# Performance work log

Hardware: AMD Instinct MI355X
Metric: run time of the kernel (lower is better)

The kernel has to match this reference:

```python
import jax, jax.numpy as jnp
import numpy as np
import math

B, L, E, H = 4, 2048, 1024, 16
HD = E // H
SIGMA = 10.0
ATTN_BIAS = 0.1  # source bug: dropout_p=0.1 is passed as attn_mask and added to scores


def setup_inputs() -> dict:
    key = jax.random.key(0)
    ks = jax.random.split(key, 6)
    return {
        "query": jax.random.normal(ks[0], (B, L, E), jnp.float32),
        "key": jax.random.normal(ks[1], (B, L, E), jnp.float32),
        "value": jax.random.normal(ks[2], (B, L, E), jnp.float32),
        "gauss": jax.random.uniform(ks[3], (B * H // 2, L), jnp.float32),
        "in_proj_weight": jax.random.normal(ks[4], (3 * E, E), jnp.float32) * (1.0 / math.sqrt(E)),
        "in_proj_bias": jnp.zeros((3 * E,), jnp.float32),
        "out_proj_weight": jax.random.normal(ks[5], (E, E), jnp.float32) * (1.0 / math.sqrt(E)),
        "out_proj_bias": jnp.zeros((E,), jnp.float32),
    }


def reference(query, key, value, gauss, in_proj_weight, in_proj_bias,
              out_proj_weight, out_proj_bias):
    # packed in-projection (q,k,v distinct tensors -> chunk weights in 3)
    wq, wk, wv = jnp.split(in_proj_weight, 3, axis=0)   # each [E, E]
    bq, bk, bv = jnp.split(in_proj_bias, 3, axis=0)
    q = query @ wq.T + bq          # [B, L, E]
    k = key @ wk.T + bk
    v = value @ wv.T + bv

    def split_heads(x):            # [B, L, E] -> [B*H, L, HD], index = b*H + h
        return x.reshape(B, L, H, HD).transpose(0, 2, 1, 3).reshape(B * H, L, HD)

    q, k, v = split_heads(q), split_heads(k), split_heads(v)
    q = q * (1.0 / math.sqrt(HD))

    attn = jnp.einsum("bnd,bmd->bnm", q, k) + ATTN_BIAS   # [B*H, L, L]
    gw = jnp.exp(-gauss * SIGMA)                          # [B*H//2, L]
    # even/odd batch rows share the same gaussian row -> pairwise broadcast
    attn = (attn.reshape(B * H // 2, 2, L, L) * gw[:, None, None, :]).reshape(B * H, L, L)
    attn = jax.nn.softmax(attn, axis=-1)

    out = jnp.einsum("bnm,bmd->bnd", attn, v)             # [B*H, L, HD]
    out = out.reshape(B, H, L, HD).transpose(0, 2, 1, 3).reshape(B, L, E)
    return out @ out_proj_weight.T + out_proj_bias        # [B, L, E]
```

## Files before the change

kernel.cpp:

```cpp
#include <hip/hip_runtime.h>
#include <stdint.h>
#include <stddef.h>


typedef __attribute__((ext_vector_type(8))) short bf16x8;
typedef __attribute__((ext_vector_type(4))) float f32x4;
typedef __attribute__((ext_vector_type(8))) float f32x8;

__device__ __forceinline__ unsigned short f2b(float f) {
  unsigned int u = __builtin_bit_cast(unsigned int, f);
  u += 0x7FFFu + ((u >> 16) & 1u);
  return (unsigned short)(u >> 16);
}
__device__ __forceinline__ bf16x8 cvt8(f32x4 a, f32x4 b) {
  bf16x8 r;
#pragma unroll
  for (int i = 0; i < 4; ++i) { r[i] = (short)f2b(a[i]); r[4 + i] = (short)f2b(b[i]); }
  return r;
}
__device__ __forceinline__ bf16x8 pk8(f32x4 a, f32x4 b) {
  union { bf16x8 v; unsigned int w[4]; } u;
  asm("v_cvt_pk_bf16_f32 %0, %1, %2" : "=v"(u.w[0]) : "v"(a[0]), "v"(a[1]));
  asm("v_cvt_pk_bf16_f32 %0, %1, %2" : "=v"(u.w[1]) : "v"(a[2]), "v"(a[3]));
  asm("v_cvt_pk_bf16_f32 %0, %1, %2" : "=v"(u.w[2]) : "v"(b[0]), "v"(b[1]));
  asm("v_cvt_pk_bf16_f32 %0, %1, %2" : "=v"(u.w[3]) : "v"(b[2]), "v"(b[3]));
  return u.v;
}
__device__ __forceinline__ float fexp2(float x) { return __builtin_amdgcn_exp2f(x); }

#define GLD16(gp, lp) __builtin_amdgcn_global_load_lds( \
  (const __attribute__((address_space(1))) void*)(gp), \
  (__attribute__((address_space(3))) void*)(lp), 16, 0, 0)

__global__ void __launch_bounds__(256) gw_exp_kernel(const float* __restrict__ g,
                                                     float* __restrict__ gw2, int n) {
  int i = blockIdx.x * 256 + threadIdx.x;
  if (i < n) {
    const float e = __expf(g[i] * -10.0f) * 1.44269504f;
    gw2[2 * i] = e;
    gw2[2 * i + 1] = 0.1f * e;
  }
}

__global__ void __launch_bounds__(256) conv_bf16_kernel(
    const float* __restrict__ q, const float* __restrict__ k, const float* __restrict__ v,
    const float* __restrict__ w1, const float* __restrict__ w2,
    unsigned short* __restrict__ dst)
{
  const size_t i = ((size_t)blockIdx.x * 256 + threadIdx.x) * 8;
  const int seg = (int)(i >> 20);
  const float* s; size_t off;
  if (seg < 8)       { s = q;  off = i; }
  else if (seg < 16) { s = k;  off = i - ((size_t)8 << 20); }
  else if (seg < 24) { s = v;  off = i - ((size_t)16 << 20); }
  else if (seg < 27) { s = w1; off = i - ((size_t)24 << 20); }
  else               { s = w2; off = i - ((size_t)27 << 20); }
  const f32x4 a = *(const f32x4*)(s + off);
  const f32x4 b = *(const f32x4*)(s + off + 4);
  *(bf16x8*)(dst + i) = cvt8(a, b);
}

template<int EPI>
__global__ void __launch_bounds__(256) gemm_bt(
    const unsigned short* __restrict__ A0, const unsigned short* __restrict__ Bw,
    const float* __restrict__ bias,
    unsigned short* __restrict__ Qo, unsigned short* __restrict__ Ko,
    unsigned short* __restrict__ Vto, float* __restrict__ Co,
    int N, int K, int nTN)
{
  const int nwg = gridDim.x;
  const int cpx = nwg >> 3;
  const int bid2 = (blockIdx.x & 7) * cpx + (blockIdx.x >> 3);
  const int tm = bid2 / nTN, tn = bid2 % nTN;

  const unsigned short* A = A0;
  if (EPI == 0) A = A0 + (size_t)(tn >> 3) * 8388608;

  __shared__ __align__(16) char ldsA[3][8192];
  __shared__ __align__(16) char ldsB[3][8192];

  const int tid = threadIdx.x;
  const int w = tid >> 6, l = tid & 63;
  const int lr = l & 15, lg = l >> 4;
  const size_t Kz = (size_t)K;

  auto stage = [&](int buf, int kt) {
    const int k0 = kt * 32;
    const int rl = l >> 2;
    const int cs = (l & 3) ^ ((l >> 3) & 3);
#pragma unroll
    for (int i = 0; i < 2; ++i) {
      const int s = i * 4 + w;
      const size_t row = (size_t)(s * 16 + rl);
      GLD16(A  + (Kz * (tm * 128 + row)) + k0 + cs * 8, &ldsA[buf][s * 1024]);
      GLD16(Bw + (Kz * (tn * 128 + row)) + k0 + cs * 8, &ldsB[buf][s * 1024]);
    }
  };

  auto loadFrag = [&](const char* ld, int row) -> bf16x8 {
    return *(const bf16x8*)(ld + row * 64 + ((lg ^ ((row >> 1) & 3)) << 4));
  };

  f32x4 acc[4][4];
  const f32x4 zero = {0.f, 0.f, 0.f, 0.f};
#pragma unroll
  for (int i = 0; i < 4; ++i)
#pragma unroll
    for (int j = 0; j < 4; ++j) acc[i][j] = zero;

  const int wr = (w >> 1) * 64, wc = (w & 1) * 64;
  const int NT = K / 32;

  stage(0, 0);
  stage(1, 1);
  int rb = 0, wb = 2;
  for (int kt = 0; kt < NT; ++kt) {
    if (kt == NT - 1) { asm volatile("s_waitcnt vmcnt(0)" ::: "memory"); }
    else              { asm volatile("s_waitcnt vmcnt(4)" ::: "memory"); }
    __builtin_amdgcn_sched_barrier(0);
    __builtin_amdgcn_s_barrier();
    __builtin_amdgcn_sched_barrier(0);
    if (kt + 2 < NT) stage(wb, kt + 2);
    const char* la = ldsA[rb];
    const char* lb = ldsB[rb];
    bf16x8 af[4], bfr[4];
#pragma unroll
    for (int mi = 0; mi < 4; ++mi) af[mi] = loadFrag(la, wr + mi * 16 + lr);
#pragma unroll
    for (int ni = 0; ni < 4; ++ni) bfr[ni] = loadFrag(lb, wc + ni * 16 + lr);
#pragma unroll
    for (int mi = 0; mi < 4; ++mi)
#pragma unroll
      for (int ni = 0; ni < 4; ++ni)
        acc[mi][ni] = __builtin_amdgcn_mfma_f32_16x16x32_bf16(
            af[mi], bfr[ni], acc[mi][ni], 0, 0, 0);
    rb = (rb == 2) ? 0 : rb + 1;
    wb = (wb == 2) ? 0 : wb + 1;
  }

#pragma unroll
  for (int ni = 0; ni < 4; ++ni) {
    const int cn = tn * 128 + wc + ni * 16 + lr;
    const float bv = bias[cn];
#pragma unroll
    for (int mi = 0; mi < 4; ++mi) {
#pragma unroll
      for (int r = 0; r < 4; ++r) {
        const int rm = tm * 128 + wr + mi * 16 + lg * 4 + r;
        const float val = acc[mi][ni][r] + bv;
        if constexpr (EPI == 0) {
          const int which = cn >> 10;
          const int j = cn & 1023;
          const int bh = (rm >> 11) * 16 + (j >> 6);
          const int d = j & 63;
          const int n = rm & 2047;
          if (which == 0)      Qo[((size_t)bh * 2048 + n) * 64 + d] = f2b(val * 0.125f);
          else if (which == 1) Ko[((size_t)bh * 2048 + n) * 64 + d] = f2b(val);
          else                 Vto[((size_t)bh * 64 + d) * 2048 + n] = f2b(val);
        } else {
          Co[(size_t)rm * N + cn] = val;
        }
      }
    }
  }
}

__global__ void __launch_bounds__(256, 4) attn_kernel(
    const unsigned short* __restrict__ Q, const unsigned short* __restrict__ Kf,
    const unsigned short* __restrict__ Vt, const float* __restrict__ gw2,
    unsigned short* __restrict__ O)
{
  const int bh = blockIdx.x >> 4;
  const int qb = blockIdx.x & 15;
  const int tid = threadIdx.x;
  const int w = tid >> 6, l = tid & 63;
  const int lr = l & 15, lg = l >> 4;

  __shared__ __align__(16) unsigned short Kl[2][64 * 64];
  __shared__ __align__(16) unsigned short Vl[2][64 * 64];

  const int qrow = qb * 128 + w * 32 + lr;
  const unsigned short* qp = &Q[((size_t)bh * 2048 + qrow) * 64];
  const bf16x8 aqA0 = *(const bf16x8*)&qp[lg * 8];
  const bf16x8 aqA1 = *(const bf16x8*)&qp[32 + lg * 8];
  const bf16x8 aqB0 = *(const bf16x8*)&qp[16 * 64 + lg * 8];
  const bf16x8 aqB1 = *(const bf16x8*)&qp[16 * 64 + 32 + lg * 8];

  const f32x4 zero = {0.f, 0.f, 0.f, 0.f};
  f32x4 accOA[4], accOB[4], lA = zero, lB = zero;
#pragma unroll
  for (int dt = 0; dt < 4; ++dt) { accOA[dt] = zero; accOB[dt] = zero; }

  const short oneb = (short)0x3F80;
  const bf16x8 vones = {oneb, oneb, oneb, oneb, oneb, oneb, oneb, oneb};

  int off[4][2];
#pragma unroll
  for (int mt = 0; mt < 4; ++mt)
#pragma unroll
    for (int c = 0; c < 2; ++c) {
      const int rr = mt * 16 + lr;
      off[mt][c] = rr * 128 + ((((c << 2) + lg) ^ (rr & 7)) << 4);
    }

  const int rr0 = w * 8 + (l >> 3);
  const int cc = ((l & 7) ^ (rr0 & 7)) * 8;
  const int kk0 = (rr0 & 35) | ((rr0 & 12) << 1) | ((rr0 & 16) >> 2);
  const unsigned short* kSrc = &Kf[((size_t)bh * 2048 + kk0) * 64 + cc];
  const unsigned short* vSrc = &Vt[((size_t)bh * 64 + rr0) * 2048 + cc];

  auto stageKV = [&](int buf) {
    GLD16(kSrc,             &Kl[buf][w * 512]);
    GLD16(kSrc + 32 * 64,   &Kl[buf][(w + 4) * 512]);
    GLD16(vSrc,             &Vl[buf][w * 512]);
    GLD16(vSrc + 32 * 2048, &Vl[buf][(w + 4) * 512]);
    kSrc += 64 * 64;
    vSrc += 64;
  };

  const float* gwrow = &gw2[(size_t)(bh >> 1) * 4096];

  stageKV(0);
  for (int t = 0; t < 32; ++t) {
    __syncthreads();
    if (t + 1 < 32) stageKV((t + 1) & 1);
    const char* kl = (const char*)Kl[t & 1];
    const char* vl = (const char*)Vl[t & 1];

    f32x4 s0[4], s1[4];
    __builtin_amdgcn_s_setprio(1);
#pragma unroll
    for (int mt = 0; mt < 4; ++mt) {
      f32x4 a0 = zero, a1 = zero;
#pragma unroll
      for (int dk = 0; dk < 2; ++dk) {
        const bf16x8 bk = *(const bf16x8*)(kl + off[mt][dk]);
        a0 = __builtin_amdgcn_mfma_f32_16x16x32_bf16(bk, dk ? aqA1 : aqA0, a0, 0, 0, 0);
        a1 = __builtin_amdgcn_mfma_f32_16x16x32_bf16(bk, dk ? aqB1 : aqB0, a1, 0, 0, 0);
      }
      const f32x8 g8 = *(const f32x8*)(gwrow + ((t << 7) + ((mt >> 1) << 6) + ((mt & 1) << 3) + (lg << 4)));
#pragma unroll
      for (int r = 0; r < 4; ++r) {
        s0[mt][r] = __builtin_fmaf(a0[r], g8[2 * r], g8[2 * r + 1]);
        s1[mt][r] = __builtin_fmaf(a1[r], g8[2 * r], g8[2 * r + 1]);
      }
    }
    __builtin_amdgcn_s_setprio(0);

#pragma unroll
    for (int mt = 0; mt < 4; ++mt)
#pragma unroll
      for (int r = 0; r < 4; ++r) {
        s0[mt][r] = fexp2(s0[mt][r]);
        s1[mt][r] = fexp2(s1[mt][r]);
      }
    const bf16x8 apA0 = pk8(s0[0], s0[1]);
    const bf16x8 apA1 = pk8(s0[2], s0[3]);
    const bf16x8 apB0 = pk8(s1[0], s1[1]);
    const bf16x8 apB1 = pk8(s1[2], s1[3]);

    __builtin_amdgcn_s_setprio(1);
    lA = __builtin_amdgcn_mfma_f32_16x16x32_bf16(apA0, vones, lA, 0, 0, 0);
    lA = __builtin_amdgcn_mfma_f32_16x16x32_bf16(apA1, vones, lA, 0, 0, 0);
    lB = __builtin_amdgcn_mfma_f32_16x16x32_bf16(apB0, vones, lB, 0, 0, 0);
    lB = __builtin_amdgcn_mfma_f32_16x16x32_bf16(apB1, vones, lB, 0, 0, 0);

#pragma unroll
    for (int dt = 0; dt < 4; ++dt) {
      f32x4 a = accOA[dt], b = accOB[dt];
#pragma unroll
      for (int ms = 0; ms < 2; ++ms) {
        const bf16x8 bv = *(const bf16x8*)(vl + off[dt][ms]);
        a = __builtin_amdgcn_mfma_f32_16x16x32_bf16(ms ? apA1 : apA0, bv, a, 0, 0, 0);
        b = __builtin_amdgcn_mfma_f32_16x16x32_bf16(ms ? apB1 : apB0, bv, b, 0, 0, 0);
      }
      accOA[dt] = a; accOB[dt] = b;
    }
    __builtin_amdgcn_s_setprio(0);
  }

  const int orowA = (bh >> 4) * 2048 + qb * 128 + w * 32 + lg * 4;
  const int oc0 = (bh & 15) * 64;
  f32x4 rA, rB;
#pragma unroll
  for (int r = 0; r < 4; ++r) { rA[r] = 1.0f / lA[r]; rB[r] = 1.0f / lB[r]; }
#pragma unroll
  for (int dt = 0; dt < 4; ++dt) {
#pragma unroll
    for (int r = 0; r < 4; ++r) {
      O[(size_t)(orowA + r) * 1024 + oc0 + dt * 16 + lr]      = f2b(accOA[dt][r] * rA[r]);
      O[(size_t)(orowA + 16 + r) * 1024 + oc0 + dt * 16 + lr] = f2b(accOB[dt][r] * rB[r]);
    }
  }
}

extern "C" void kernel_launch(void* const* d_in, const int* in_sizes, int n_in,
                              void* d_out, int out_size, void* d_ws, size_t ws_size,
                              hipStream_t stream) {
  (void)in_sizes; (void)n_in; (void)out_size; (void)ws_size;
  const float* query = (const float*)d_in[0];
  const float* key_  = (const float*)d_in[1];
  const float* value = (const float*)d_in[2];
  const float* gauss = (const float*)d_in[3];
  const float* ipw   = (const float*)d_in[4];
  const float* ipb   = (const float*)d_in[5];
  const float* opw   = (const float*)d_in[6];
  const float* opb   = (const float*)d_in[7];

  char* ws = (char*)d_ws;
  unsigned short* Xbf = (unsigned short*)ws;
  unsigned short* W1  = Xbf + ((size_t)24 << 20);
  unsigned short* W2  = Xbf + ((size_t)27 << 20);
  unsigned short* AO  = Xbf;
  unsigned short* Qf  = Xbf + ((size_t)28 << 20);
  unsigned short* Kf  = Qf + (size_t)64 * 2048 * 64;
  unsigned short* Vt  = Kf + (size_t)64 * 2048 * 64;
  float*          gw2 = (float*)(Vt + (size_t)64 * 2048 * 64);

  gw_exp_kernel<<<256, 256, 0, stream>>>(gauss, gw2, 32 * 2048);

  conv_bf16_kernel<<<14336, 256, 0, stream>>>(query, key_, value, ipw, opw, Xbf);

  gemm_bt<0><<<64 * 24, 256, 0, stream>>>(
      Xbf, W1, ipb, Qf, Kf, Vt, nullptr, 3072, 1024, 24);

  attn_kernel<<<64 * 16, 256, 0, stream>>>(Qf, Kf, Vt, gw2, AO);

  gemm_bt<1><<<64 * 8, 256, 0, stream>>>(
      AO, W2, opb, nullptr, nullptr, nullptr, (float*)d_out, 1024, 1024, 8);
}
```

Before: 230.8 us.

## Use 512-thread GEMM blocks and stage V-transpose epilogue through LDS

The projection GEMMs now launch 512 threads (8 waves) per 128x128 tile, so each wave computes a 64x32 sub-tile and issues one global-to-LDS load per operand per stage instead of two. A and B tiles share a single LDS array. For the V part of the input projection, the epilogue writes bias-added bf16 results transposed into swizzled LDS, then emits coalesced 16-byte stores to the transposed V layout in place of scattered 2-byte strided stores. The tradeoff is fewer accumulators per wave and less fragment reuse, plus extra barriers in the V epilogue.

```diff
diff --git a/kernel.cpp b/kernel.cpp
--- a/kernel.cpp
+++ b/kernel.cpp
@@ -61,7 +61,7 @@
 }
 
 template<int EPI>
-__global__ void __launch_bounds__(256) gemm_bt(
+__global__ void __launch_bounds__(512) gemm_bt(
     const unsigned short* __restrict__ A0, const unsigned short* __restrict__ Bw,
     const float* __restrict__ bias,
     unsigned short* __restrict__ Qo, unsigned short* __restrict__ Ko,
@@ -76,8 +76,7 @@
   const unsigned short* A = A0;
   if (EPI == 0) A = A0 + (size_t)(tn >> 3) * 8388608;
 
-  __shared__ __align__(16) char ldsA[3][8192];
-  __shared__ __align__(16) char ldsB[3][8192];
+  __shared__ __align__(16) char lds[3][16384];
 
   const int tid = threadIdx.x;
   const int w = tid >> 6, l = tid & 63;
@@ -88,27 +87,23 @@
     const int k0 = kt * 32;
     const int rl = l >> 2;
     const int cs = (l & 3) ^ ((l >> 3) & 3);
-#pragma unroll
-    for (int i = 0; i < 2; ++i) {
-      const int s = i * 4 + w;
-      const size_t row = (size_t)(s * 16 + rl);
-      GLD16(A  + (Kz * (tm * 128 + row)) + k0 + cs * 8, &ldsA[buf][s * 1024]);
-      GLD16(Bw + (Kz * (tn * 128 + row)) + k0 + cs * 8, &ldsB[buf][s * 1024]);
-    }
+    const size_t row = (size_t)(w * 16 + rl);
+    GLD16(A  + Kz * (tm * 128 + row) + k0 + cs * 8, &lds[buf][w * 1024]);
+    GLD16(Bw + Kz * (tn * 128 + row) + k0 + cs * 8, &lds[buf][8192 + w * 1024]);
   };
 
   auto loadFrag = [&](const char* ld, int row) -> bf16x8 {
     return *(const bf16x8*)(ld + row * 64 + ((lg ^ ((row >> 1) & 3)) << 4));
   };
 
-  f32x4 acc[4][4];
+  f32x4 acc[4][2];
   const f32x4 zero = {0.f, 0.f, 0.f, 0.f};
 #pragma unroll
   for (int i = 0; i < 4; ++i)
 #pragma unroll
-    for (int j = 0; j < 4; ++j) acc[i][j] = zero;
-
-  const int wr = (w >> 1) * 64, wc = (w & 1) * 64;
+    for (int j = 0; j < 2; ++j) acc[i][j] = zero;
+
+  const int wr = (w >> 2) * 64, wc = (w & 3) * 32;
   const int NT = K / 32;
 
   stage(0, 0);
@@ -116,49 +111,79 @@
   int rb = 0, wb = 2;
   for (int kt = 0; kt < NT; ++kt) {
     if (kt == NT - 1) { asm volatile("s_waitcnt vmcnt(0)" ::: "memory"); }
-    else              { asm volatile("s_waitcnt vmcnt(4)" ::: "memory"); }
+    else              { asm volatile("s_waitcnt vmcnt(2)" ::: "memory"); }
     __builtin_amdgcn_sched_barrier(0);
     __builtin_amdgcn_s_barrier();
     __builtin_amdgcn_sched_barrier(0);
     if (kt + 2 < NT) stage(wb, kt + 2);
-    const char* la = ldsA[rb];
-    const char* lb = ldsB[rb];
-    bf16x8 af[4], bfr[4];
+    const char* la = lds[rb];
+    const char* lb = lds[rb] + 8192;
+    bf16x8 af[4], bfr[2];
 #pragma unroll
     for (int mi = 0; mi < 4; ++mi) af[mi] = loadFrag(la, wr + mi * 16 + lr);
 #pragma unroll
-    for (int ni = 0; ni < 4; ++ni) bfr[ni] = loadFrag(lb, wc + ni * 16 + lr);
+    for (int ni = 0; ni < 2; ++ni) bfr[ni] = loadFrag(lb, wc + ni * 16 + lr);
 #pragma unroll
     for (int mi = 0; mi < 4; ++mi)
 #pragma unroll
-      for (int ni = 0; ni < 4; ++ni)
+      for (int ni = 0; ni < 2; ++ni)
         acc[mi][ni] = __builtin_amdgcn_mfma_f32_16x16x32_bf16(
             af[mi], bfr[ni], acc[mi][ni], 0, 0, 0);
     rb = (rb == 2) ? 0 : rb + 1;
     wb = (wb == 2) ? 0 : wb + 1;
   }
 
-#pragma unroll
-  for (int ni = 0; ni < 4; ++ni) {
-    const int cn = tn * 128 + wc + ni * 16 + lr;
-    const float bv = bias[cn];
-#pragma unroll
-    for (int mi = 0; mi < 4; ++mi) {
-#pragma unroll
-      for (int r = 0; r < 4; ++r) {
-        const int rm = tm * 128 + wr + mi * 16 + lg * 4 + r;
-        const float val = acc[mi][ni][r] + bv;
-        if constexpr (EPI == 0) {
-          const int which = cn >> 10;
-          const int j = cn & 1023;
-          const int bh = (rm >> 11) * 16 + (j >> 6);
-          const int d = j & 63;
-          const int n = rm & 2047;
-          if (which == 0)      Qo[((size_t)bh * 2048 + n) * 64 + d] = f2b(val * 0.125f);
-          else if (which == 1) Ko[((size_t)bh * 2048 + n) * 64 + d] = f2b(val);
-          else                 Vto[((size_t)bh * 64 + d) * 2048 + n] = f2b(val);
-        } else {
-          Co[(size_t)rm * N + cn] = val;
+  if (EPI == 0 && tn >= 16) {
+    __syncthreads();
+    char* T = &lds[0][0];
+#pragma unroll
+    for (int ni = 0; ni < 2; ++ni) {
+      const int cnl = wc + ni * 16 + lr;
+      const float bv = bias[tn * 128 + cnl];
+#pragma unroll
+      for (int mi = 0; mi < 4; ++mi)
+#pragma unroll
+        for (int r = 0; r < 4; ++r) {
+          const int rml = wr + mi * 16 + lg * 4 + r;
+          const int byte = cnl * 256 + (((rml * 2)) ^ ((cnl & 3) << 5));
+          *(unsigned short*)(T + byte) = f2b(acc[mi][ni][r] + bv);
+        }
+    }
+    __syncthreads();
+    const int bbase = (tm >> 4) * 16 + (tn - 16) * 2;
+    const size_t ncol = (size_t)(tm & 15) * 128;
+#pragma unroll
+    for (int rep = 0; rep < 4; ++rep) {
+      const int U = rep * 512 + tid;
+      const int row = U >> 4;
+      const int un = U & 15;
+      const bf16x8 vv = *(const bf16x8*)(T + row * 256 + ((un * 16) ^ ((row & 3) << 5)));
+      const int bh = bbase + (row >> 6);
+      const int d = row & 63;
+      *(bf16x8*)(Vto + ((size_t)bh * 64 + d) * 2048 + ncol + un * 8) = vv;
+    }
+  } else {
+#pragma unroll
+    for (int ni = 0; ni < 2; ++ni) {
+      const int cn = tn * 128 + wc + ni * 16 + lr;
+      const float bv = bias[cn];
+#pragma unroll
+      for (int mi = 0; mi < 4; ++mi) {
+#pragma unroll
+        for (int r = 0; r < 4; ++r) {
+          const int rm = tm * 128 + wr + mi * 16 + lg * 4 + r;
+          const float val = acc[mi][ni][r] + bv;
+          if constexpr (EPI == 0) {
+            const int which = cn >> 10;
+            const int j = cn & 1023;
+            const int bh = (rm >> 11) * 16 + (j >> 6);
+            const int d = j & 63;
+            const int n = rm & 2047;
+            if (which == 0) Qo[((size_t)bh * 2048 + n) * 64 + d] = f2b(val * 0.125f);
+            else            Ko[((size_t)bh * 2048 + n) * 64 + d] = f2b(val);
+          } else {
+            Co[(size_t)rm * N + cn] = val;
+          }
         }
       }
     }
@@ -321,11 +346,11 @@
 
   conv_bf16_kernel<<<14336, 256, 0, stream>>>(query, key_, value, ipw, opw, Xbf);
 
-  gemm_bt<0><<<64 * 24, 256, 0, stream>>>(
+  gemm_bt<0><<<64 * 24, 512, 0, stream>>>(
       Xbf, W1, ipb, Qf, Kf, Vt, nullptr, 3072, 1024, 24);
 
   attn_kernel<<<64 * 16, 256, 0, stream>>>(Qf, Kf, Vt, gw2, AO);
 
-  gemm_bt<1><<<64 * 8, 256, 0, stream>>>(
+  gemm_bt<1><<<64 * 8, 512, 0, stream>>>(
       AO, W2, opb, nullptr, nullptr, nullptr, (float*)d_out, 1024, 1024, 8);
 }
```

Result: faster. 210.5 us (-8.8%).
